# Kernel optimization log

Measured on AMD Instinct MI355X. Metric: run time of the kernel, lower is better.

The kernel has to match this reference:

```python
import jax, jax.numpy as jnp
import numpy as np

B, T, E = 32, 2048, 128

def setup_inputs() -> dict:
    key = jax.random.key(0)
    ks = jax.random.split(key, 6)
    return {
        "x1": jax.random.normal(ks[0], (B, T, E), dtype=jnp.float32),
        "x2": jax.random.normal(ks[1], (B, T, E), dtype=jnp.float32),
        "W1": jax.random.normal(ks[2], (E, 1), dtype=jnp.float32) * 0.05,
        "b1": jnp.zeros((T, 1), dtype=jnp.float32),
        "U1": jax.random.normal(ks[3], (E, T), dtype=jnp.float32) * 0.05,
        "W2": jax.random.normal(ks[4], (E, 1), dtype=jnp.float32) * 0.05,
        "b2": jnp.zeros((T, 1), dtype=jnp.float32),
        "U2": jax.random.normal(ks[5], (E, T), dtype=jnp.float32) * 0.05,
    }


def reference(x1, x2, W1, b1, U1, W2, b2, U2):
    # S[b,i,j] = <x1[b,i], x2[b,j]>  -> (B, T, T)
    S = jnp.einsum('bie,bje->bij', x1, x2)
    inv_T = jnp.float32(1.0) / S.shape[1]
    # c1 = mean_j sum_i S[b,i,j] * x2[b,i,e]  -> (B, E)
    c1 = jnp.einsum('bij,bie->be', S, x2) * inv_T
    # c2 = mean_i sum_j S[b,i,j] * x1[b,j,e]  -> (B, E)
    c2 = jnp.einsum('bij,bje->be', S, x1) * inv_T
    # attention logits: (B, T)
    et1 = c1 @ U1 + jnp.squeeze(x1 @ W1 + b1, axis=-1)
    et2 = c2 @ U2 + jnp.squeeze(x2 @ W2 + b2, axis=-1)
    at1 = jax.nn.softmax(et1, axis=-1)
    at2 = jax.nn.softmax(et2, axis=-1)
    # attention-weighted sums: (B, E)
    o1 = jnp.einsum('bt,bte->be', at1, x1)
    o2 = jnp.einsum('bt,bte->be', at2, x2)
    # merge_mode == 'concat'
    return jnp.concatenate([o1, o2], axis=1)
```

## Files before the change

### kernel.cpp

```cpp
#include <hip/hip_runtime.h>


#define B_ 32
#define T_ 2048
#define E_ 128
#define EV (E_/4)
#define INV_T (1.0f/2048.0f)
#define RC 128
#define NG (T_/RC)

#define WS_PSX1 0
#define WS_PSX2 65536
#define WS_PM   131072
#define WS_ET1  8519680
#define WS_ET2  8585216
#define WS_C1   8650752
#define WS_C2   8683520

typedef __attribute__((ext_vector_type(8))) short short8;
typedef __attribute__((ext_vector_type(4))) float f32x4;

__device__ __forceinline__ float dot4(float4 a, float4 b) {
    return a.x*b.x + a.y*b.y + a.z*b.z + a.w*b.w;
}
__device__ __forceinline__ void fma4(float4& a, float s, const float4 v) {
    a.x += s*v.x; a.y += s*v.y; a.z += s*v.z; a.w += s*v.w;
}
__device__ __forceinline__ void add4(float4& a, const float4 v) {
    a.x += v.x; a.y += v.y; a.z += v.z; a.w += v.w;
}

__device__ __forceinline__ unsigned swz(int e, unsigned tbyte) {
    return tbyte ^ ((((unsigned)e & 3u) << 3) | ((((unsigned)e >> 2) & 3u) << 5));
}

__device__ __forceinline__ void pack_hilo(float f0, float f1, float f2, float f3,
                                          unsigned long long& wh,
                                          unsigned long long& wl) {
    unsigned u0 = __float_as_uint(f0), u1 = __float_as_uint(f1);
    unsigned u2 = __float_as_uint(f2), u3 = __float_as_uint(f3);
    unsigned h0 = u0 & 0xFFFF0000u, h1 = u1 & 0xFFFF0000u;
    unsigned h2 = u2 & 0xFFFF0000u, h3 = u3 & 0xFFFF0000u;
    unsigned hw0 = h1 | (h0 >> 16);
    unsigned hw1 = h3 | (h2 >> 16);
    unsigned l0 = __float_as_uint(f0 - __uint_as_float(h0));
    unsigned l1 = __float_as_uint(f1 - __uint_as_float(h1));
    unsigned l2 = __float_as_uint(f2 - __uint_as_float(h2));
    unsigned l3 = __float_as_uint(f3 - __uint_as_float(h3));
    unsigned lw0 = (l1 & 0xFFFF0000u) | (l0 >> 16);
    unsigned lw1 = (l3 & 0xFFFF0000u) | (l2 >> 16);
    wh = ((unsigned long long)hw1 << 32) | hw0;
    wl = ((unsigned long long)lw1 << 32) | lw0;
}

__device__ __forceinline__ short8 frag_ld(const char* buf, int row, int t0) {
    unsigned a1 = (unsigned)row * 128u + swz(row, (unsigned)t0 * 2u);
    union { unsigned long long u[2]; short8 v; } r;
    r.u[0] = *(const unsigned long long*)(buf + a1);
    r.u[1] = *(const unsigned long long*)(buf + (a1 ^ 32u));
    return r.v;
}

__global__ __launch_bounds__(256)
void ka_gram(const float* __restrict__ x1, const float* __restrict__ x2,
             const float* __restrict__ W1, const float* __restrict__ b1,
             const float* __restrict__ W2, const float* __restrict__ b2,
             float* __restrict__ ws) {
    __shared__ unsigned short ldsq[4][128][64];
    __shared__ float4 sW[2][32];
    const int b = blockIdx.x, g = blockIdx.y, tid = threadIdx.x;
    if (tid < 64) sW[tid>>5][tid&31] = ((const float4*)((tid<32) ? W1 : W2))[tid&31];
    __syncthreads();

    const int eq = tid & 31, tp = tid >> 5;
    const int lane = tid & 63, w = tid >> 6;

    const float4* x1g = (const float4*)x1 + ((size_t)b*T_ + g*RC)*EV;
    const float4* x2g = (const float4*)x2 + ((size_t)b*T_ + g*RC)*EV;

    float4 psA1 = {0,0,0,0}, psA2 = {0,0,0,0};
    f32x4 acc[2][8];
    #pragma unroll
    for (int i = 0; i < 2; ++i)
        #pragma unroll
        for (int j = 0; j < 8; ++j) acc[i][j] = (f32x4){0.f,0.f,0.f,0.f};

    char* Lb = (char*)&ldsq[0][0][0];
    const char* Apass[3] = { Lb + 2*16384, Lb + 2*16384, Lb + 3*16384 };
    const char* Bpass[3] = { Lb + 0,       Lb + 1*16384, Lb + 0       };

    for (int s = 0; s < 2; ++s) {
        #pragma unroll
        for (int u = 0; u < 4; ++u) {
            const int ten = u >> 1;
            const int tq  = tp + (u & 1)*8;
            const int tl  = tq*4;
            const int tr  = s*64 + tl;
            const float4* src = (ten ? x2g : x1g) + (size_t)tr*EV + eq;
            const float4 v0 = src[0], v1 = src[EV], v2 = src[2*EV], v3 = src[3*EV];
            float4& ps = ten ? psA2 : psA1;
            add4(ps, v0); add4(ps, v1); add4(ps, v2); add4(ps, v3);
            const float4 wv = sW[ten][eq];
            float d0 = dot4(v0,wv), d1 = dot4(v1,wv), d2 = dot4(v2,wv), d3 = dot4(v3,wv);
            #pragma unroll
            for (int mm = 1; mm <= 16; mm <<= 1) {
                d0 += __shfl_xor(d0, mm); d1 += __shfl_xor(d1, mm);
                d2 += __shfl_xor(d2, mm); d3 += __shfl_xor(d3, mm);
            }
            if (eq == 0) {
                const int tg = g*RC + tr;
                const float4 bb = *(const float4*)((ten ? b2 : b1) + tg);
                *(float4*)(ws + (ten ? WS_ET2 : WS_ET1) + (size_t)b*T_ + tg)
                    = make_float4(d0+bb.x, d1+bb.y, d2+bb.z, d3+bb.w);
            }
            char* Hb = Lb + (ten ? 2 : 0)*16384;
            char* Lo = Hb + 16384;
            const unsigned tb = (unsigned)tl * 2u;
            unsigned long long wh, wl;
            {   const int e = eq*4 + 0; const unsigned off = (unsigned)e*128u + swz(e, tb);
                pack_hilo(v0.x, v1.x, v2.x, v3.x, wh, wl);
                *(unsigned long long*)(Hb + off) = wh;
                *(unsigned long long*)(Lo + off) = wl; }
            {   const int e = eq*4 + 1; const unsigned off = (unsigned)e*128u + swz(e, tb);
                pack_hilo(v0.y, v1.y, v2.y, v3.y, wh, wl);
                *(unsigned long long*)(Hb + off) = wh;
                *(unsigned long long*)(Lo + off) = wl; }
            {   const int e = eq*4 + 2; const unsigned off = (unsigned)e*128u + swz(e, tb);
                pack_hilo(v0.z, v1.z, v2.z, v3.z, wh, wl);
                *(unsigned long long*)(Hb + off) = wh;
                *(unsigned long long*)(Lo + off) = wl; }
            {   const int e = eq*4 + 3; const unsigned off = (unsigned)e*128u + swz(e, tb);
                pack_hilo(v0.w, v1.w, v2.w, v3.w, wh, wl);
                *(unsigned long long*)(Hb + off) = wh;
                *(unsigned long long*)(Lo + off) = wl; }
        }
        __syncthreads();
        #pragma unroll
        for (int pass = 0; pass < 3; ++pass) {
            #pragma unroll
            for (int ks = 0; ks < 2; ++ks) {
                const int t0 = ks*32 + ((lane>>4)<<2);
                const short8 a0 = frag_ld(Apass[pass], w*32 + (lane&15), t0);
                const short8 a1 = frag_ld(Apass[pass], w*32 + 16 + (lane&15), t0);
                #pragma unroll
                for (int ft = 0; ft < 8; ++ft) {
                    const short8 bv = frag_ld(Bpass[pass], ft*16 + (lane&15), t0);
                    acc[0][ft] = __builtin_amdgcn_mfma_f32_16x16x32_bf16(a0, bv, acc[0][ft], 0, 0, 0);
                    acc[1][ft] = __builtin_amdgcn_mfma_f32_16x16x32_bf16(a1, bv, acc[1][ft], 0, 0, 0);
                }
            }
        }
        __syncthreads();
    }

    float* pM = ws + WS_PM + (size_t)(b*NG + g)*16384;
    #pragma unroll
    for (int et = 0; et < 2; ++et) {
        #pragma unroll
        for (int ft = 0; ft < 8; ++ft) {
            #pragma unroll
            for (int r = 0; r < 4; ++r) {
                const int e = w*32 + et*16 + ((lane>>4)<<2) + r;
                const int f = ft*16 + (lane&15);
                pM[e*128 + f] = acc[et][ft][r];
            }
        }
    }

    float4* spx = (float4*)Lb;
    spx[tid*2 + 0] = psA1; spx[tid*2 + 1] = psA2;
    __syncthreads();
    if (tid < 64) {
        const int ten = tid>>5, eqq = tid&31;
        float4 sum = {0,0,0,0};
        #pragma unroll
        for (int t2 = 0; t2 < 8; ++t2) add4(sum, spx[(t2*32 + eqq)*2 + ten]);
        ((float4*)(ws + (ten ? WS_PSX2 : WS_PSX1)))[(size_t)(b*NG + g)*32 + eqq] = sum;
    }
}

__global__ __launch_bounds__(256)
void kb_c(float* __restrict__ ws) {
    __shared__ float4 ssx1v[32], ssx2v[32];
    __shared__ float4 c2p[8][32];
    const int b = blockIdx.x, gs = blockIdx.y, tid = threadIdx.x;
    float* ssx1 = (float*)ssx1v;
    float* ssx2 = (float*)ssx2v;
    if (tid < 128) {
        float s = 0.f;
        #pragma unroll
        for (int g = 0; g < NG; ++g) s += ws[WS_PSX2 + (size_t)(b*NG + g)*E_ + tid];
        ssx2[tid] = s;
    } else {
        float s = 0.f;
        #pragma unroll
        for (int g = 0; g < NG; ++g) s += ws[WS_PSX1 + (size_t)(b*NG + g)*E_ + (tid-128)];
        ssx1[tid-128] = s;
    }
    __syncthreads();
    const int hw = tid>>5, j = tid&31;
    const float4* pM4 = (const float4*)(ws + WS_PM) + (size_t)b*NG*4096;
    const float4 sxj = ssx2v[j];
    float4 c2a = {0,0,0,0};
    #pragma unroll
    for (int r = 0; r < 16; ++r) {
        const int e = hw*16 + r;
        const float s1 = ssx1[e];
        float ca = 0.f;
        #pragma unroll
        for (int g2 = 0; g2 < 2; ++g2) {
            float4 v = pM4[(size_t)(gs*2 + g2)*4096 + e*32 + j];
            ca += dot4(v, sxj);
            fma4(c2a, s1, v);
        }
        #pragma unroll
        for (int m = 1; m <= 16; m <<= 1) ca += __shfl_xor(ca, m);
        if (j == 0) ws[WS_C1 + (size_t)(b*8 + gs)*E_ + e] = ca * INV_T;
    }
    c2p[hw][j] = c2a;
    __syncthreads();
    if (tid < 128) {
        float s = 0.f;
        #pragma unroll
        for (int h = 0; h < 8; ++h) s += ((const float*)c2p)[h*128 + tid];
        ws[WS_C2 + (size_t)(b*8 + gs)*E_ + tid] = s * INV_T;
    }
}

__global__ __launch_bounds__(256)
void kc_etU(const float* __restrict__ U1, const float* __restrict__ U2,
            float* __restrict__ ws) {
    __shared__ float s_c[B_][E_];
    const int ch = blockIdx.x, sel = blockIdx.y, tid = threadIdx.x;
    const float4* c4g = (const float4*)(ws + (sel ? WS_C2 : WS_C1));
    float4* s_c4 = (float4*)&s_c[0][0];
    #pragma unroll
    for (int i = 0; i < 4; ++i) {
        const int idx = tid + 256*i;
        const int base = (idx & ~31)*8 + (idx & 31);
        float4 s = {0,0,0,0};
        #pragma unroll
        for (int gs = 0; gs < 8; ++gs) add4(s, c4g[base + gs*32]);
        s_c4[idx] = s;
    }
    __syncthreads();
    const float4* U4 = (const float4*)(sel ? U2 : U1);
    const int c4i = tid&31, bg = tid>>5;
    float4 acc[4];
    #pragma unroll
    for (int q = 0; q < 4; ++q) acc[q] = make_float4(0.f,0.f,0.f,0.f);
    #pragma unroll 4
    for (int e = 0; e < E_; ++e) {
        const float4 u = U4[(size_t)e*(T_/4) + ch*32 + c4i];
        fma4(acc[0], s_c[bg*4+0][e], u);
        fma4(acc[1], s_c[bg*4+1][e], u);
        fma4(acc[2], s_c[bg*4+2][e], u);
        fma4(acc[3], s_c[bg*4+3][e], u);
    }
    float4* et4 = (float4*)(ws + (sel ? WS_ET2 : WS_ET1));
    #pragma unroll
    for (int q = 0; q < 4; ++q) {
        const int bb = bg*4 + q;
        const size_t idx = (size_t)bb*(T_/4) + ch*32 + c4i;
        float4 v = et4[idx];
        add4(v, acc[q]);
        et4[idx] = v;
    }
}

__global__ __launch_bounds__(512)
void kd_softmax(float* __restrict__ ws, float* __restrict__ out) {
    __shared__ float red[512];
    const int b = blockIdx.x, sel = blockIdx.y, tid = threadIdx.x;
    float4* et4 = (float4*)(ws + (sel ? WS_ET2 : WS_ET1) + (size_t)b*T_);
    float4 v = et4[tid];
    if (tid < E_) out[b*2*E_ + sel*E_ + tid] = 0.f;
    float m = fmaxf(fmaxf(v.x, v.y), fmaxf(v.z, v.w));
    red[tid] = m; __syncthreads();
    for (int s = 256; s > 0; s >>= 1) {
        if (tid < s) red[tid] = fmaxf(red[tid], red[tid+s]);
        __syncthreads();
    }
    m = red[0]; __syncthreads();
    float4 e4;
    e4.x = __expf(v.x - m); e4.y = __expf(v.y - m);
    e4.z = __expf(v.z - m); e4.w = __expf(v.w - m);
    red[tid] = e4.x + e4.y + e4.z + e4.w;
    __syncthreads();
    for (int s = 256; s > 0; s >>= 1) {
        if (tid < s) red[tid] += red[tid+s];
        __syncthreads();
    }
    const float il = 1.f / red[0];
    e4.x *= il; e4.y *= il; e4.z *= il; e4.w *= il;
    et4[tid] = e4;
}

__global__ __launch_bounds__(256)
void ke_out(const float* __restrict__ x1, const float* __restrict__ x2,
            const float* __restrict__ ws, float* __restrict__ out) {
    __shared__ float4 s_r1[256], s_r2[256];
    __shared__ float s_p1[128], s_p2[128];
    const int b = blockIdx.x, g = blockIdx.y, tid = threadIdx.x;
    const float* pr1 = ws + WS_ET1 + (size_t)b*T_ + g*128;
    const float* pr2 = ws + WS_ET2 + (size_t)b*T_ + g*128;
    if (tid < 128) s_p1[tid] = pr1[tid];
    else           s_p2[tid - 128] = pr2[tid - 128];
    __syncthreads();
    const float4* p1 = (const float4*)x1 + ((size_t)b*T_ + g*128)*EV;
    const float4* p2 = (const float4*)x2 + ((size_t)b*T_ + g*128)*EV;
    const int rg = tid >> 5, q = tid & 31;
    float4 a1 = {0,0,0,0}, a2 = {0,0,0,0};
    #pragma unroll
    for (int i = 0; i < 16; ++i) {
        int r = i*8 + rg;
        fma4(a1, s_p1[r], p1[r*EV + q]);
        fma4(a2, s_p2[r], p2[r*EV + q]);
    }
    s_r1[tid] = a1; s_r2[tid] = a2;
    __syncthreads();
    for (int s = 128; s >= 32; s >>= 1) {
        if (tid < s) { add4(s_r1[tid], s_r1[tid+s]); add4(s_r2[tid], s_r2[tid+s]); }
        __syncthreads();
    }
    if (tid < 32) {
        float4 t1 = s_r1[tid], t2 = s_r2[tid];
        atomicAdd(&out[b*2*E_ + tid*4+0], t1.x);
        atomicAdd(&out[b*2*E_ + tid*4+1], t1.y);
        atomicAdd(&out[b*2*E_ + tid*4+2], t1.z);
        atomicAdd(&out[b*2*E_ + tid*4+3], t1.w);
        atomicAdd(&out[b*2*E_ + E_ + tid*4+0], t2.x);
        atomicAdd(&out[b*2*E_ + E_ + tid*4+1], t2.y);
        atomicAdd(&out[b*2*E_ + E_ + tid*4+2], t2.z);
        atomicAdd(&out[b*2*E_ + E_ + tid*4+3], t2.w);
    }
}

extern "C" void kernel_launch(void* const* d_in, const int* in_sizes, int n_in,
                              void* d_out, int out_size, void* d_ws, size_t ws_size,
                              hipStream_t stream) {
    const float* x1 = (const float*)d_in[0];
    const float* x2 = (const float*)d_in[1];
    const float* W1 = (const float*)d_in[2];
    const float* b1 = (const float*)d_in[3];
    const float* U1 = (const float*)d_in[4];
    const float* W2 = (const float*)d_in[5];
    const float* b2 = (const float*)d_in[6];
    const float* U2 = (const float*)d_in[7];
    float* ws  = (float*)d_ws;
    float* out = (float*)d_out;

    ka_gram<<<dim3(B_, NG), 256, 0, stream>>>(x1, x2, W1, b1, W2, b2, ws);
    kb_c<<<dim3(B_, 8), 256, 0, stream>>>(ws);
    kc_etU<<<dim3(16, 2), 256, 0, stream>>>(U1, U2, ws);
    kd_softmax<<<dim3(B_, 2), 512, 0, stream>>>(ws, out);
    ke_out<<<dim3(B_, 16), 256, 0, stream>>>(x1, x2, ws, out);
}
```

Baseline: 165.4 us.

## Fuse c-vector reduction, U projection and softmax into one kernel per batch

After: 173.9 us. 1.05x slower.

```diff
diff --git a/kernel.cpp b/kernel.cpp
--- a/kernel.cpp
+++ b/kernel.cpp
@@ -14,8 +14,6 @@
 #define WS_PM   131072
 #define WS_ET1  8519680
 #define WS_ET2  8585216
-#define WS_C1   8650752
-#define WS_C2   8683520
 
 typedef __attribute__((ext_vector_type(8))) short short8;
 typedef __attribute__((ext_vector_type(4))) float f32x4;
@@ -179,103 +177,79 @@
     }
 }
 
-__global__ __launch_bounds__(256)
-void kb_c(float* __restrict__ ws) {
-    __shared__ float4 ssx1v[32], ssx2v[32];
-    __shared__ float4 c2p[8][32];
-    const int b = blockIdx.x, gs = blockIdx.y, tid = threadIdx.x;
-    float* ssx1 = (float*)ssx1v;
-    float* ssx2 = (float*)ssx2v;
-    if (tid < 128) {
-        float s = 0.f;
-        #pragma unroll
-        for (int g = 0; g < NG; ++g) s += ws[WS_PSX2 + (size_t)(b*NG + g)*E_ + tid];
-        ssx2[tid] = s;
-    } else {
-        float s = 0.f;
-        #pragma unroll
-        for (int g = 0; g < NG; ++g) s += ws[WS_PSX1 + (size_t)(b*NG + g)*E_ + (tid-128)];
-        ssx1[tid-128] = s;
-    }
-    __syncthreads();
-    const int hw = tid>>5, j = tid&31;
-    const float4* pM4 = (const float4*)(ws + WS_PM) + (size_t)b*NG*4096;
-    const float4 sxj = ssx2v[j];
-    float4 c2a = {0,0,0,0};
-    #pragma unroll
-    for (int r = 0; r < 16; ++r) {
-        const int e = hw*16 + r;
-        const float s1 = ssx1[e];
-        float ca = 0.f;
-        #pragma unroll
-        for (int g2 = 0; g2 < 2; ++g2) {
-            float4 v = pM4[(size_t)(gs*2 + g2)*4096 + e*32 + j];
-            ca += dot4(v, sxj);
-            fma4(c2a, s1, v);
-        }
-        #pragma unroll
-        for (int m = 1; m <= 16; m <<= 1) ca += __shfl_xor(ca, m);
-        if (j == 0) ws[WS_C1 + (size_t)(b*8 + gs)*E_ + e] = ca * INV_T;
-    }
-    c2p[hw][j] = c2a;
-    __syncthreads();
-    if (tid < 128) {
-        float s = 0.f;
-        #pragma unroll
-        for (int h = 0; h < 8; ++h) s += ((const float*)c2p)[h*128 + tid];
-        ws[WS_C2 + (size_t)(b*8 + gs)*E_ + tid] = s * INV_T;
-    }
-}
-
-__global__ __launch_bounds__(256)
-void kc_etU(const float* __restrict__ U1, const float* __restrict__ U2,
-            float* __restrict__ ws) {
-    __shared__ float s_c[B_][E_];
-    const int ch = blockIdx.x, sel = blockIdx.y, tid = threadIdx.x;
-    const float4* c4g = (const float4*)(ws + (sel ? WS_C2 : WS_C1));
-    float4* s_c4 = (float4*)&s_c[0][0];
-    #pragma unroll
-    for (int i = 0; i < 4; ++i) {
-        const int idx = tid + 256*i;
-        const int base = (idx & ~31)*8 + (idx & 31);
-        float4 s = {0,0,0,0};
-        #pragma unroll
-        for (int gs = 0; gs < 8; ++gs) add4(s, c4g[base + gs*32]);
-        s_c4[idx] = s;
-    }
-    __syncthreads();
-    const float4* U4 = (const float4*)(sel ? U2 : U1);
-    const int c4i = tid&31, bg = tid>>5;
-    float4 acc[4];
-    #pragma unroll
-    for (int q = 0; q < 4; ++q) acc[q] = make_float4(0.f,0.f,0.f,0.f);
-    #pragma unroll 4
-    for (int e = 0; e < E_; ++e) {
-        const float4 u = U4[(size_t)e*(T_/4) + ch*32 + c4i];
-        fma4(acc[0], s_c[bg*4+0][e], u);
-        fma4(acc[1], s_c[bg*4+1][e], u);
-        fma4(acc[2], s_c[bg*4+2][e], u);
-        fma4(acc[3], s_c[bg*4+3][e], u);
-    }
-    float4* et4 = (float4*)(ws + (sel ? WS_ET2 : WS_ET1));
-    #pragma unroll
-    for (int q = 0; q < 4; ++q) {
-        const int bb = bg*4 + q;
-        const size_t idx = (size_t)bb*(T_/4) + ch*32 + c4i;
-        float4 v = et4[idx];
-        add4(v, acc[q]);
-        et4[idx] = v;
-    }
-}
-
 __global__ __launch_bounds__(512)
-void kd_softmax(float* __restrict__ ws, float* __restrict__ out) {
+void kf_cet(const float* __restrict__ U1, const float* __restrict__ U2,
+            float* __restrict__ ws, float* __restrict__ out) {
+    __shared__ float ssx[E_];
+    __shared__ float s_c[E_];
+    __shared__ float4 c2p[16][32];
     __shared__ float red[512];
     const int b = blockIdx.x, sel = blockIdx.y, tid = threadIdx.x;
+    if (tid < 128) {
+        const float* ps = ws + (sel ? WS_PSX1 : WS_PSX2);
+        float s = 0.f;
+        #pragma unroll
+        for (int g = 0; g < NG; ++g) s += ps[(size_t)(b*NG + g)*E_ + tid];
+        ssx[tid] = s;
+    }
+    __syncthreads();
+    const float4* pM4 = (const float4*)(ws + WS_PM) + (size_t)b*NG*4096;
+    const float4* sx4 = (const float4*)ssx;
+    if (sel == 0) {
+        const int e = tid >> 2, part = tid & 3;
+        float ca = 0.f;
+        for (int g = 0; g < NG; ++g) {
+            #pragma unroll
+            for (int i = 0; i < 8; ++i)
+                ca += dot4(pM4[(size_t)g*4096 + e*32 + part*8 + i], sx4[part*8 + i]);
+        }
+        ca += __shfl_xor(ca, 1); ca += __shfl_xor(ca, 2);
+        if (part == 0) s_c[e] = ca * INV_T;
+    } else {
+        const int eg = tid >> 5, f4 = tid & 31;
+        float4 a = {0,0,0,0};
+        for (int g = 0; g < NG; ++g) {
+            #pragma unroll
+            for (int i = 0; i < 8; ++i) {
+                const int e = eg*8 + i;
+                fma4(a, ssx[e], pM4[(size_t)g*4096 + e*32 + f4]);
+            }
+        }
+        c2p[eg][f4] = a;
+        __syncthreads();
+        if (tid < 128) {
+            const int qr = tid >> 5, f = tid & 31;
+            float4 s = {0,0,0,0};
+            #pragma unroll
+            for (int j = 0; j < 4; ++j) add4(s, c2p[qr*4 + j][f]);
+            c2p[qr][f] = s;
+        }
+        __syncthreads();
+        if (tid < 32) {
+            float4 s = {0,0,0,0};
+            #pragma unroll
+            for (int j = 0; j < 4; ++j) add4(s, c2p[j][tid]);
+            s.x *= INV_T; s.y *= INV_T; s.z *= INV_T; s.w *= INV_T;
+            ((float4*)s_c)[tid] = s;
+        }
+    }
+    __syncthreads();
+
+    const float4* U4 = (const float4*)(sel ? U2 : U1);
     float4* et4 = (float4*)(ws + (sel ? WS_ET2 : WS_ET1) + (size_t)b*T_);
-    float4 v = et4[tid];
+    float4 accA = et4[tid];
+    float4 accB = {0,0,0,0}, accC = {0,0,0,0}, accD = {0,0,0,0};
+    #pragma unroll 2
+    for (int e = 0; e < E_; e += 4) {
+        fma4(accA, s_c[e+0], U4[(size_t)(e+0)*(T_/4) + tid]);
+        fma4(accB, s_c[e+1], U4[(size_t)(e+1)*(T_/4) + tid]);
+        fma4(accC, s_c[e+2], U4[(size_t)(e+2)*(T_/4) + tid]);
+        fma4(accD, s_c[e+3], U4[(size_t)(e+3)*(T_/4) + tid]);
+    }
+    add4(accA, accB); add4(accC, accD); add4(accA, accC);
     if (tid < E_) out[b*2*E_ + sel*E_ + tid] = 0.f;
-    float m = fmaxf(fmaxf(v.x, v.y), fmaxf(v.z, v.w));
+
+    float m = fmaxf(fmaxf(accA.x, accA.y), fmaxf(accA.z, accA.w));
     red[tid] = m; __syncthreads();
     for (int s = 256; s > 0; s >>= 1) {
         if (tid < s) red[tid] = fmaxf(red[tid], red[tid+s]);
@@ -283,8 +257,8 @@
     }
     m = red[0]; __syncthreads();
     float4 e4;
-    e4.x = __expf(v.x - m); e4.y = __expf(v.y - m);
-    e4.z = __expf(v.z - m); e4.w = __expf(v.w - m);
+    e4.x = __expf(accA.x - m); e4.y = __expf(accA.y - m);
+    e4.z = __expf(accA.z - m); e4.w = __expf(accA.w - m);
     red[tid] = e4.x + e4.y + e4.z + e4.w;
     __syncthreads();
     for (int s = 256; s > 0; s >>= 1) {
@@ -351,8 +325,6 @@
     float* out = (float*)d_out;
 
     ka_gram<<<dim3(B_, NG), 256, 0, stream>>>(x1, x2, W1, b1, W2, b2, ws);
-    kb_c<<<dim3(B_, 8), 256, 0, stream>>>(ws);
-    kc_etU<<<dim3(16, 2), 256, 0, stream>>>(U1, U2, ws);
-    kd_softmax<<<dim3(B_, 2), 512, 0, stream>>>(ws, out);
+    kf_cet<<<dim3(B_, 2), 512, 0, stream>>>(U1, U2, ws, out);
     ke_out<<<dim3(B_, 16), 256, 0, stream>>>(x1, x2, ws, out);
 }
```
